# Kernel tuning notes

Measured on AMD Instinct MI355X. Metric: run time of the kernel, lower is better.

Reference implementation:

```python
import jax, jax.numpy as jnp
import numpy as np

N = 100_000      # nodes
E = 1_600_000    # edges
DIN = 128
DH = 128
DOUT = 2
BN_EPS = 1e-5


def setup_inputs() -> dict:
    key = jax.random.key(0)
    ks = jax.random.split(key, 14)
    s_in = 1.0 / np.sqrt(DIN)
    s_h = 1.0 / np.sqrt(DH)
    return {
        "x": jax.random.normal(ks[0], (N, DIN), jnp.float32),
        "edge_index": jax.random.randint(ks[1], (2, E), 0, N, jnp.int32),
        "W1": jax.random.normal(ks[2], (DIN, DH), jnp.float32) * s_in,
        "b1": jnp.zeros((DH,), jnp.float32),
        "W2": jax.random.normal(ks[3], (DH, DH), jnp.float32) * s_h,
        "b2": jnp.zeros((DH,), jnp.float32),
        "W3": jax.random.normal(ks[4], (DH, DH), jnp.float32) * s_h,
        "b3": jnp.zeros((DH,), jnp.float32),
        "gamma": jnp.ones((DH,), jnp.float32),
        "beta": jnp.zeros((DH,), jnp.float32),
        "Wc": jax.random.normal(ks[5], (DH, DH), jnp.float32) * s_h,
        "bc": jnp.zeros((DH,), jnp.float32),
        "Wr": jax.random.normal(ks[6], (DH, DOUT), jnp.float32) * s_h,
        "br": jnp.zeros((DOUT,), jnp.float32),
    }


def reference(x, edge_index, W1, b1, W2, b2, W3, b3, gamma, beta, Wc, bc, Wr, br):
    src, dst = edge_index[0], edge_index[1]
    # GCN symmetric normalization with self-loops (deg includes self-loop)
    deg = jnp.zeros((N,), x.dtype).at[dst].add(1.0) + 1.0
    dinv = jax.lax.rsqrt(deg)
    coef = (dinv[src] * dinv[dst])[:, None]        # [E,1]
    self_coef = (dinv * dinv)[:, None]             # [N,1] self-loop weight

    def gcn_conv(h, W, b):
        h = h @ W                                  # [N,DH] dense transform
        agg = jnp.zeros((N, h.shape[1]), h.dtype).at[dst].add(h[src] * coef)
        return agg + h * self_coef + b

    h = jax.nn.relu(gcn_conv(x, W1, b1))
    h = jax.nn.relu(gcn_conv(h, W2, b2))   # dropout is identity at inference
    h = jax.nn.relu(gcn_conv(h, W3, b3))
    # BatchNorm1d over the node dimension (training-mode batch statistics)
    mu = h.mean(axis=0)
    var = h.var(axis=0)
    h = (h - mu) * jax.lax.rsqrt(var + BN_EPS) * gamma + beta
    h = jax.nn.relu(h @ Wc + bc)
    return h @ Wr + br
```

## Files before the change

kernel.cpp:

```cpp
#include <hip/hip_runtime.h>

#define DHC 128
#define BSHIFT 8
#define BSIZE 256

typedef __attribute__((ext_vector_type(8))) __bf16 bf16x8;
typedef __attribute__((ext_vector_type(8))) unsigned short ushort8;
typedef __attribute__((ext_vector_type(4))) float floatx4;

__device__ inline unsigned short f2bf(float f) {
    unsigned int u = __float_as_uint(f);
    return (unsigned short)((u + 0x7FFFu + ((u >> 16) & 1u)) >> 16);
}
__device__ inline float bf2f_lo(unsigned int v) { return __uint_as_float(v << 16); }
__device__ inline float bf2f_hi(unsigned int v) { return __uint_as_float(v & 0xFFFF0000u); }


__global__ __launch_bounds__(256) void bucket_hist(const int* __restrict__ dst,
                                                   int* __restrict__ bcount, int e) {
    __shared__ int h[512];
    for (int i = threadIdx.x; i < 512; i += 256) h[i] = 0;
    __syncthreads();
    int base = blockIdx.x * 4096 + threadIdx.x;
#pragma unroll
    for (int j = 0; j < 16; j++) {
        int i = base + j * 256;
        if (i < e) atomicAdd(&h[dst[i] >> BSHIFT], 1);
    }
    __syncthreads();
    for (int i = threadIdx.x; i < 512; i += 256)
        if (h[i]) atomicAdd(&bcount[i], h[i]);
}

__global__ void bucket_scan(const int* __restrict__ bcount, int* __restrict__ bbase,
                            int* __restrict__ bcur, int* __restrict__ row_ptr,
                            int nb, int n, int e) {
    __shared__ int s[512];
    int t = threadIdx.x;
    s[t] = (t < nb) ? bcount[t] : 0;
    __syncthreads();
    for (int off = 1; off < 512; off <<= 1) {
        int add = (t >= off) ? s[t - off] : 0;
        __syncthreads();
        s[t] += add;
        __syncthreads();
    }
    if (t < nb) {
        int ex = (t == 0) ? 0 : s[t - 1];
        bbase[t] = ex;
        bcur[t] = ex;
    }
    if (t == 0) {
        bbase[nb] = e;
        row_ptr[n] = e;
    }
}

__global__ __launch_bounds__(256) void bucket_scatter(const int* __restrict__ src,
                                                      const int* __restrict__ dst,
                                                      int* __restrict__ bcur,
                                                      unsigned int* __restrict__ ebuf, int e) {
    __shared__ int h[512];
    __shared__ int rsv[512];
    for (int i = threadIdx.x; i < 512; i += 256) h[i] = 0;
    __syncthreads();
    int base = blockIdx.x * 4096 + threadIdx.x;
    int sreg[16], dreg[16];
#pragma unroll
    for (int j = 0; j < 16; j++) {
        int i = base + j * 256;
        if (i < e) {
            sreg[j] = src[i];
            dreg[j] = dst[i];
            atomicAdd(&h[dreg[j] >> BSHIFT], 1);
        } else {
            dreg[j] = -1;
        }
    }
    __syncthreads();
    for (int i = threadIdx.x; i < 512; i += 256) {
        int c = h[i];
        rsv[i] = c ? atomicAdd(&bcur[i], c) : 0;
        h[i] = 0;
    }
    __syncthreads();
#pragma unroll
    for (int j = 0; j < 16; j++) {
        if (dreg[j] >= 0) {
            int b = dreg[j] >> BSHIFT;
            int pos = rsv[b] + atomicAdd(&h[b], 1);
            ebuf[pos] = (unsigned int)sreg[j] | ((unsigned int)(dreg[j] & (BSIZE - 1)) << 20);
        }
    }
}

__global__ __launch_bounds__(256) void bucket_build(const unsigned int* __restrict__ ebuf,
                                                    const int* __restrict__ bbase,
                                                    int* __restrict__ row_ptr,
                                                    int* __restrict__ csr_src,
                                                    float* __restrict__ dinv,
                                                    float* __restrict__ selfc, int n) {
    __shared__ int ldeg[256];
    __shared__ int lcur[256];
    int b = blockIdx.x;
    int t = threadIdx.x;
    int beg = bbase[b], end = bbase[b + 1];
    ldeg[t] = 0;
    __syncthreads();
    for (int i = beg + t; i < end; i += 256) atomicAdd(&ldeg[ebuf[i] >> 20], 1);
    __syncthreads();
    int deg = ldeg[t];
    lcur[t] = deg;
    __syncthreads();
    for (int off = 1; off < 256; off <<= 1) {
        int add = (t >= off) ? lcur[t - off] : 0;
        __syncthreads();
        lcur[t] += add;
        __syncthreads();
    }
    int rp = beg + lcur[t] - deg;
    int node = (b << BSHIFT) + t;
    if (node < n) {
        row_ptr[node] = rp;
        float dv = rsqrtf((float)(deg + 1));
        dinv[node] = dv;
        selfc[node] = dv * dv;
    }
    __syncthreads();
    lcur[t] = rp;
    __syncthreads();
    for (int i = beg + t; i < end; i += 256) {
        unsigned int p = ebuf[i];
        int pos = atomicAdd(&lcur[p >> 20], 1);
        csr_src[pos] = (int)(p & 0xFFFFFu);
    }
}

__global__ void wconv3_k(const float* __restrict__ W1, const float* __restrict__ W2,
                         const float* __restrict__ W3, unsigned short* __restrict__ WTall) {
    int idx = blockIdx.x * 256 + threadIdx.x;
    int wsel = idx >> 14;
    int i = idx & 16383;
    int nn = i >> 7, k = i & 127;
    const float* W = (wsel == 0) ? W1 : (wsel == 1) ? W2 : W3;
    WTall[idx] = f2bf(W[k * 128 + nn]);
}

template <int MODE, int AF32>
__global__ __launch_bounds__(256, 2) void gemm_k(const void* __restrict__ Avoid,
                                                 const unsigned short* __restrict__ WT,
                                                 const float* __restrict__ bias,
                                                 unsigned short* __restrict__ outB,
                                                 float* __restrict__ outF,
                                                 const float* __restrict__ Wr,
                                                 const float* __restrict__ br, int n) {
    const int wave = threadIdx.x >> 6;
    const int lane = threadIdx.x & 63;
    const int m = lane & 15;
    const int kq = lane >> 4;

    bf16x8 bfrag[4][8];
#pragma unroll
    for (int ks = 0; ks < 4; ks++) {
        const int kb = ks * 32 + kq * 8;
#pragma unroll
        for (int ct = 0; ct < 8; ct++) {
            int nn = ct * 16 + m;
            bfrag[ks][ct] = __builtin_bit_cast(bf16x8, *(const ushort8*)(WT + nn * 128 + kb));
        }
    }

    const int rowbase = (blockIdx.x * 4 + wave) * 32;
    const int r0 = min(rowbase + m, n - 1);
    const int r1 = min(rowbase + 16 + m, n - 1);

    floatx4 acc[2][8];
#pragma unroll
    for (int rt = 0; rt < 2; rt++)
#pragma unroll
        for (int ct = 0; ct < 8; ct++) acc[rt][ct] = (floatx4){0.f, 0.f, 0.f, 0.f};

#pragma unroll
    for (int ks = 0; ks < 4; ks++) {
        const int kb = ks * 32 + kq * 8;
        bf16x8 a0, a1;
        if (AF32) {
            const float* Af = (const float*)Avoid;
            float4 f00 = *(const float4*)(Af + (size_t)r0 * 128 + kb);
            float4 f01 = *(const float4*)(Af + (size_t)r0 * 128 + kb + 4);
            float4 f10 = *(const float4*)(Af + (size_t)r1 * 128 + kb);
            float4 f11 = *(const float4*)(Af + (size_t)r1 * 128 + kb + 4);
            ushort8 u0, u1;
            u0[0] = f2bf(f00.x); u0[1] = f2bf(f00.y); u0[2] = f2bf(f00.z); u0[3] = f2bf(f00.w);
            u0[4] = f2bf(f01.x); u0[5] = f2bf(f01.y); u0[6] = f2bf(f01.z); u0[7] = f2bf(f01.w);
            u1[0] = f2bf(f10.x); u1[1] = f2bf(f10.y); u1[2] = f2bf(f10.z); u1[3] = f2bf(f10.w);
            u1[4] = f2bf(f11.x); u1[5] = f2bf(f11.y); u1[6] = f2bf(f11.z); u1[7] = f2bf(f11.w);
            a0 = __builtin_bit_cast(bf16x8, u0);
            a1 = __builtin_bit_cast(bf16x8, u1);
        } else {
            const unsigned short* Ab = (const unsigned short*)Avoid;
            a0 = __builtin_bit_cast(bf16x8, *(const ushort8*)(Ab + (size_t)r0 * 128 + kb));
            a1 = __builtin_bit_cast(bf16x8, *(const ushort8*)(Ab + (size_t)r1 * 128 + kb));
        }
#pragma unroll
        for (int ct = 0; ct < 8; ct++) {
            acc[0][ct] = __builtin_amdgcn_mfma_f32_16x16x32_bf16(a0, bfrag[ks][ct], acc[0][ct], 0, 0, 0);
            acc[1][ct] = __builtin_amdgcn_mfma_f32_16x16x32_bf16(a1, bfrag[ks][ct], acc[1][ct], 0, 0, 0);
        }
    }

    if (MODE == 0) {
#pragma unroll
        for (int rt = 0; rt < 2; rt++) {
#pragma unroll
            for (int ct = 0; ct < 8; ct++) {
                int col = ct * 16 + m;
#pragma unroll
                for (int i = 0; i < 4; i++) {
                    int r = rowbase + rt * 16 + kq * 4 + i;
                    if (r < n) outB[(size_t)r * 128 + col] = f2bf(acc[rt][ct][i]);
                }
            }
        }
    } else {
        float bcv[8], wr0[8], wr1[8];
#pragma unroll
        for (int ct = 0; ct < 8; ct++) {
            int col = ct * 16 + m;
            bcv[ct] = bias[col];
            float2 wv = ((const float2*)Wr)[col];
            wr0[ct] = wv.x;
            wr1[ct] = wv.y;
        }
        float br0 = br[0], br1 = br[1];
#pragma unroll
        for (int rt = 0; rt < 2; rt++) {
#pragma unroll
            for (int i = 0; i < 4; i++) {
                float p0 = 0.f, p1 = 0.f;
#pragma unroll
                for (int ct = 0; ct < 8; ct++) {
                    float v = fmaxf(acc[rt][ct][i] + bcv[ct], 0.f);
                    p0 = fmaf(v, wr0[ct], p0);
                    p1 = fmaf(v, wr1[ct], p1);
                }
#pragma unroll
                for (int mk = 1; mk < 16; mk <<= 1) {
                    p0 += __shfl_xor(p0, mk);
                    p1 += __shfl_xor(p1, mk);
                }
                int r = rowbase + rt * 16 + kq * 4 + i;
                if (m == 0 && r < n) ((float2*)outF)[r] = make_float2(p0 + br0, p1 + br1);
            }
        }
    }
}

__global__ __launch_bounds__(256) void agg_k(const unsigned short* __restrict__ hW,
                                             const int* __restrict__ csr,
                                             const int* __restrict__ row_ptr,
                                             const float* __restrict__ dinv,
                                             const float* __restrict__ selfc,
                                             const float* __restrict__ bias,
                                             unsigned short* __restrict__ out, int n) {
    int node = blockIdx.x * 4 + (threadIdx.x >> 6);
    int lane = threadIdx.x & 63;
    if (node >= n) return;
    int g = lane >> 4, t = lane & 15;
    int beg = row_ptr[node], end = row_ptr[node + 1];
    float dd = dinv[node];
    const uint4* h4 = (const uint4*)hW;
    float a[8];
#pragma unroll
    for (int i = 0; i < 8; i++) a[i] = 0.f;

    int len = end - beg;
    int q = (len + 3) >> 2;
    int e = beg + g * q;
    int e1 = min(e + q, end);

    for (; e + 3 < e1; e += 4) {
        int s0 = csr[e + 0], s1 = csr[e + 1], s2 = csr[e + 2], s3 = csr[e + 3];
        float c0 = dinv[s0] * dd, c1 = dinv[s1] * dd, c2 = dinv[s2] * dd, c3 = dinv[s3] * dd;
        uint4 v0 = h4[(size_t)s0 * 16 + t];
        uint4 v1 = h4[(size_t)s1 * 16 + t];
        uint4 v2 = h4[(size_t)s2 * 16 + t];
        uint4 v3 = h4[(size_t)s3 * 16 + t];
        a[0] = fmaf(c0, bf2f_lo(v0.x), a[0]); a[1] = fmaf(c0, bf2f_hi(v0.x), a[1]);
        a[2] = fmaf(c0, bf2f_lo(v0.y), a[2]); a[3] = fmaf(c0, bf2f_hi(v0.y), a[3]);
        a[4] = fmaf(c0, bf2f_lo(v0.z), a[4]); a[5] = fmaf(c0, bf2f_hi(v0.z), a[5]);
        a[6] = fmaf(c0, bf2f_lo(v0.w), a[6]); a[7] = fmaf(c0, bf2f_hi(v0.w), a[7]);
        a[0] = fmaf(c1, bf2f_lo(v1.x), a[0]); a[1] = fmaf(c1, bf2f_hi(v1.x), a[1]);
        a[2] = fmaf(c1, bf2f_lo(v1.y), a[2]); a[3] = fmaf(c1, bf2f_hi(v1.y), a[3]);
        a[4] = fmaf(c1, bf2f_lo(v1.z), a[4]); a[5] = fmaf(c1, bf2f_hi(v1.z), a[5]);
        a[6] = fmaf(c1, bf2f_lo(v1.w), a[6]); a[7] = fmaf(c1, bf2f_hi(v1.w), a[7]);
        a[0] = fmaf(c2, bf2f_lo(v2.x), a[0]); a[1] = fmaf(c2, bf2f_hi(v2.x), a[1]);
        a[2] = fmaf(c2, bf2f_lo(v2.y), a[2]); a[3] = fmaf(c2, bf2f_hi(v2.y), a[3]);
        a[4] = fmaf(c2, bf2f_lo(v2.z), a[4]); a[5] = fmaf(c2, bf2f_hi(v2.z), a[5]);
        a[6] = fmaf(c2, bf2f_lo(v2.w), a[6]); a[7] = fmaf(c2, bf2f_hi(v2.w), a[7]);
        a[0] = fmaf(c3, bf2f_lo(v3.x), a[0]); a[1] = fmaf(c3, bf2f_hi(v3.x), a[1]);
        a[2] = fmaf(c3, bf2f_lo(v3.y), a[2]); a[3] = fmaf(c3, bf2f_hi(v3.y), a[3]);
        a[4] = fmaf(c3, bf2f_lo(v3.z), a[4]); a[5] = fmaf(c3, bf2f_hi(v3.z), a[5]);
        a[6] = fmaf(c3, bf2f_lo(v3.w), a[6]); a[7] = fmaf(c3, bf2f_hi(v3.w), a[7]);
    }
    for (; e < e1; e++) {
        int s = csr[e];
        float c = dinv[s] * dd;
        uint4 v = h4[(size_t)s * 16 + t];
        a[0] = fmaf(c, bf2f_lo(v.x), a[0]); a[1] = fmaf(c, bf2f_hi(v.x), a[1]);
        a[2] = fmaf(c, bf2f_lo(v.y), a[2]); a[3] = fmaf(c, bf2f_hi(v.y), a[3]);
        a[4] = fmaf(c, bf2f_lo(v.z), a[4]); a[5] = fmaf(c, bf2f_hi(v.z), a[5]);
        a[6] = fmaf(c, bf2f_lo(v.w), a[6]); a[7] = fmaf(c, bf2f_hi(v.w), a[7]);
    }

    if (g == 0) {
        float sc = selfc[node];
        uint4 v = h4[(size_t)node * 16 + t];
        a[0] = fmaf(sc, bf2f_lo(v.x), a[0]); a[1] = fmaf(sc, bf2f_hi(v.x), a[1]);
        a[2] = fmaf(sc, bf2f_lo(v.y), a[2]); a[3] = fmaf(sc, bf2f_hi(v.y), a[3]);
        a[4] = fmaf(sc, bf2f_lo(v.z), a[4]); a[5] = fmaf(sc, bf2f_hi(v.z), a[5]);
        a[6] = fmaf(sc, bf2f_lo(v.w), a[6]); a[7] = fmaf(sc, bf2f_hi(v.w), a[7]);
    }
#pragma unroll
    for (int i = 0; i < 8; i++) {
        a[i] += __shfl_xor(a[i], 16);
        a[i] += __shfl_xor(a[i], 32);
    }
    if (g == 0) {
        float4 b0 = ((const float4*)bias)[t * 2];
        float4 b1 = ((const float4*)bias)[t * 2 + 1];
        uint4 o;
        o.x = (unsigned int)f2bf(fmaxf(a[0] + b0.x, 0.f)) |
              ((unsigned int)f2bf(fmaxf(a[1] + b0.y, 0.f)) << 16);
        o.y = (unsigned int)f2bf(fmaxf(a[2] + b0.z, 0.f)) |
              ((unsigned int)f2bf(fmaxf(a[3] + b0.w, 0.f)) << 16);
        o.z = (unsigned int)f2bf(fmaxf(a[4] + b1.x, 0.f)) |
              ((unsigned int)f2bf(fmaxf(a[5] + b1.y, 0.f)) << 16);
        o.w = (unsigned int)f2bf(fmaxf(a[6] + b1.z, 0.f)) |
              ((unsigned int)f2bf(fmaxf(a[7] + b1.w, 0.f)) << 16);
        ((uint4*)out)[(size_t)node * 16 + t] = o;
    }
}

__global__ __launch_bounds__(256) void bn_stats(const unsigned short* __restrict__ h,
                                                float* __restrict__ gsum,
                                                float* __restrict__ gsumsq, int n) {
    __shared__ float red[4][256];
    int l = threadIdx.x & 63;
    int rs = threadIdx.x >> 6;
    float s0 = 0.f, s1 = 0.f, q0 = 0.f, q1 = 0.f;
    for (int r = blockIdx.x * 4 + rs; r < n; r += gridDim.x * 4) {
        unsigned int v = *(const unsigned int*)(h + (size_t)r * 128 + l * 2);
        float a = bf2f_lo(v), b = bf2f_hi(v);
        s0 += a;
        s1 += b;
        q0 = fmaf(a, a, q0);
        q1 = fmaf(b, b, q1);
    }
    red[0][threadIdx.x] = s0;
    red[1][threadIdx.x] = s1;
    red[2][threadIdx.x] = q0;
    red[3][threadIdx.x] = q1;
    __syncthreads();
    if (threadIdx.x < 64) {
        float S0 = 0.f, S1 = 0.f, Q0 = 0.f, Q1 = 0.f;
#pragma unroll
        for (int j = 0; j < 4; j++) {
            S0 += red[0][j * 64 + l];
            S1 += red[1][j * 64 + l];
            Q0 += red[2][j * 64 + l];
            Q1 += red[3][j * 64 + l];
        }
        atomicAdd(&gsum[2 * l + 0], S0);
        atomicAdd(&gsum[2 * l + 1], S1);
        atomicAdd(&gsumsq[2 * l + 0], Q0);
        atomicAdd(&gsumsq[2 * l + 1], Q1);
    }
}

__global__ void bn_fold(const float* __restrict__ gsum, const float* __restrict__ gsumsq,
                        const float* __restrict__ gamma, const float* __restrict__ beta,
                        const float* __restrict__ Wc, const float* __restrict__ bc,
                        unsigned short* __restrict__ WcT, float* __restrict__ bcP, float invN) {
    __shared__ float scaleS[128], shiftS[128];
    int j = threadIdx.x;
    float mu = gsum[j] * invN;
    float var = gsumsq[j] * invN - mu * mu;
    float sc = gamma[j] * rsqrtf(var + 1e-5f);
    scaleS[j] = sc;
    shiftS[j] = beta[j] - mu * sc;
    __syncthreads();
    float accB = bc[j];
    for (int k = 0; k < 128; k++) {
        float w = Wc[k * 128 + j];
        WcT[j * 128 + k] = f2bf(scaleS[k] * w);
        accB = fmaf(shiftS[k], w, accB);
    }
    bcP[j] = accB;
}


extern "C" void kernel_launch(void* const* d_in, const int* in_sizes, int n_in,
                              void* d_out, int out_size, void* d_ws, size_t ws_size,
                              hipStream_t stream) {
    const float* x = (const float*)d_in[0];
    const int* ei = (const int*)d_in[1];
    const float* W1 = (const float*)d_in[2];
    const float* b1 = (const float*)d_in[3];
    const float* W2 = (const float*)d_in[4];
    const float* b2 = (const float*)d_in[5];
    const float* W3 = (const float*)d_in[6];
    const float* b3 = (const float*)d_in[7];
    const float* gamma = (const float*)d_in[8];
    const float* beta = (const float*)d_in[9];
    const float* Wc = (const float*)d_in[10];
    const float* bc = (const float*)d_in[11];
    const float* Wr = (const float*)d_in[12];
    const float* br = (const float*)d_in[13];
    float* out = (float*)d_out;

    const int N = in_sizes[0] / DHC;
    const int E = in_sizes[1] / 2;
    const int* srcIdx = ei;
    const int* dstIdx = ei + E;
    const int NB = (N + BSIZE - 1) >> BSHIFT;

    char* w = (char*)d_ws;
    size_t off = 0;
    auto alloc = [&](size_t bytes) -> void* {
        void* p = w + off;
        off += (bytes + 255) & ~(size_t)255;
        return p;
    };
    unsigned short* bufA = (unsigned short*)alloc((size_t)N * DHC * 2);
    unsigned short* bufB = (unsigned short*)alloc((size_t)N * DHC * 2);
    unsigned int* ebuf = (unsigned int*)alloc((size_t)E * 4);
    int* csr_src = (int*)alloc((size_t)E * 4);
    int* row_ptr = (int*)alloc((size_t)(N + 1) * 4);
    float* dinv = (float*)alloc((size_t)N * 4);
    float* selfc = (float*)alloc((size_t)N * 4);
    int* bcount = (int*)alloc(512 * 4 + 256 * 4);
    float* stats = (float*)(bcount + 512);
    float* gsum = stats;
    float* gsumsq = stats + 128;
    int* bbase = (int*)alloc(512 * 4);
    int* bcur = (int*)alloc(512 * 4);
    unsigned short* WTall = (unsigned short*)alloc((size_t)3 * 16384 * 2);
    unsigned short* WT1 = WTall;
    unsigned short* WT2 = WTall + 16384;
    unsigned short* WT3 = WTall + 32768;
    unsigned short* WcT = (unsigned short*)alloc(16384 * 2);
    float* bcP = (float*)alloc(128 * 4);
    (void)ws_size; (void)n_in; (void)out_size;

    hipMemsetAsync(bcount, 0, 512 * 4 + 256 * 4, stream);

    const int EB = (E + 4095) / 4096;
    bucket_hist<<<EB, 256, 0, stream>>>(dstIdx, bcount, E);
    bucket_scan<<<1, 512, 0, stream>>>(bcount, bbase, bcur, row_ptr, NB, N, E);
    bucket_scatter<<<EB, 256, 0, stream>>>(srcIdx, dstIdx, bcur, ebuf, E);
    bucket_build<<<NB, 256, 0, stream>>>(ebuf, bbase, row_ptr, csr_src, dinv, selfc, N);

    wconv3_k<<<192, 256, 0, stream>>>(W1, W2, W3, WTall);

    const int gemmBlocks = (N + 127) / 128;
    const int aggBlocks = (N + 3) / 4;

    gemm_k<0, 1><<<gemmBlocks, 256, 0, stream>>>(x, WT1, nullptr, bufB, nullptr, nullptr, nullptr, N);
    agg_k<<<aggBlocks, 256, 0, stream>>>(bufB, csr_src, row_ptr, dinv, selfc, b1, bufA, N);
    gemm_k<0, 0><<<gemmBlocks, 256, 0, stream>>>(bufA, WT2, nullptr, bufB, nullptr, nullptr, nullptr, N);
    agg_k<<<aggBlocks, 256, 0, stream>>>(bufB, csr_src, row_ptr, dinv, selfc, b2, bufA, N);
    gemm_k<0, 0><<<gemmBlocks, 256, 0, stream>>>(bufA, WT3, nullptr, bufB, nullptr, nullptr, nullptr, N);
    agg_k<<<aggBlocks, 256, 0, stream>>>(bufB, csr_src, row_ptr, dinv, selfc, b3, bufA, N);

    bn_stats<<<256, 256, 0, stream>>>(bufA, gsum, gsumsq, N);
    bn_fold<<<1, 128, 0, stream>>>(gsum, gsumsq, gamma, beta, Wc, bc, WcT, bcP, 1.0f / (float)N);
    gemm_k<2, 0><<<gemmBlocks, 256, 0, stream>>>(bufA, WcT, bcP, nullptr, out, Wr, br, N);
}
```

Measured before the change: 504.3 us.

## Stage GEMM weights in LDS and assign one node per 16-lane group in aggregation

The GEMM kernel no longer holds the full 128x128 weight fragment set in registers. It stages the weights in shared memory in MFMA-fragment order and reads them per k-step, which lowers register pressure so launch bounds can allow 4 blocks per CU. The aggregation kernel now processes 16 nodes per block, with each 16-lane group walking one node's whole edge list, instead of splitting each node's edges across four groups and combining them with cross-lane shuffles. This removes the shuffle reduction and the idle lanes on short rows, at the cost of longer serial loops on high-degree nodes and extra LDS traffic in the GEMM.

```diff
diff --git a/kernel.cpp b/kernel.cpp
--- a/kernel.cpp
+++ b/kernel.cpp
@@ -147,38 +147,39 @@
 }
 
 template <int MODE, int AF32>
-__global__ __launch_bounds__(256, 2) void gemm_k(const void* __restrict__ Avoid,
+__global__ __launch_bounds__(256, 4) void gemm_k(const void* __restrict__ Avoid,
                                                  const unsigned short* __restrict__ WT,
                                                  const float* __restrict__ bias,
                                                  unsigned short* __restrict__ outB,
                                                  float* __restrict__ outF,
                                                  const float* __restrict__ Wr,
                                                  const float* __restrict__ br, int n) {
+    __shared__ unsigned short Ws[32 * 512];
+    {
+        for (int c = threadIdx.x; c < 2048; c += 256) {
+            int f = c >> 6;
+            int l = c & 63;
+            int ks = f >> 3, ct = f & 7;
+            int nn = ct * 16 + (l & 15);
+            int kb = ks * 32 + (l >> 4) * 8;
+            *(uint4*)(&Ws[c * 8]) = *(const uint4*)(&WT[nn * 128 + kb]);
+        }
+    }
+    __syncthreads();
     const int wave = threadIdx.x >> 6;
     const int lane = threadIdx.x & 63;
+    const int rowbase = blockIdx.x * 128 + wave * 32;
     const int m = lane & 15;
     const int kq = lane >> 4;
 
-    bf16x8 bfrag[4][8];
-#pragma unroll
-    for (int ks = 0; ks < 4; ks++) {
-        const int kb = ks * 32 + kq * 8;
-#pragma unroll
-        for (int ct = 0; ct < 8; ct++) {
-            int nn = ct * 16 + m;
-            bfrag[ks][ct] = __builtin_bit_cast(bf16x8, *(const ushort8*)(WT + nn * 128 + kb));
-        }
-    }
-
-    const int rowbase = (blockIdx.x * 4 + wave) * 32;
+    floatx4 acc[2][8];
+#pragma unroll
+    for (int rt = 0; rt < 2; rt++)
+#pragma unroll
+        for (int ct = 0; ct < 8; ct++) acc[rt][ct] = (floatx4){0.f, 0.f, 0.f, 0.f};
+
     const int r0 = min(rowbase + m, n - 1);
     const int r1 = min(rowbase + 16 + m, n - 1);
-
-    floatx4 acc[2][8];
-#pragma unroll
-    for (int rt = 0; rt < 2; rt++)
-#pragma unroll
-        for (int ct = 0; ct < 8; ct++) acc[rt][ct] = (floatx4){0.f, 0.f, 0.f, 0.f};
 
 #pragma unroll
     for (int ks = 0; ks < 4; ks++) {
@@ -204,8 +205,10 @@
         }
 #pragma unroll
         for (int ct = 0; ct < 8; ct++) {
-            acc[0][ct] = __builtin_amdgcn_mfma_f32_16x16x32_bf16(a0, bfrag[ks][ct], acc[0][ct], 0, 0, 0);
-            acc[1][ct] = __builtin_amdgcn_mfma_f32_16x16x32_bf16(a1, bfrag[ks][ct], acc[1][ct], 0, 0, 0);
+            bf16x8 bfr = __builtin_bit_cast(bf16x8,
+                *(const ushort8*)(&Ws[(ks * 8 + ct) * 512 + lane * 8]));
+            acc[0][ct] = __builtin_amdgcn_mfma_f32_16x16x32_bf16(a0, bfr, acc[0][ct], 0, 0, 0);
+            acc[1][ct] = __builtin_amdgcn_mfma_f32_16x16x32_bf16(a1, bfr, acc[1][ct], 0, 0, 0);
         }
     }
 
@@ -263,10 +266,9 @@
                                              const float* __restrict__ selfc,
                                              const float* __restrict__ bias,
                                              unsigned short* __restrict__ out, int n) {
-    int node = blockIdx.x * 4 + (threadIdx.x >> 6);
-    int lane = threadIdx.x & 63;
+    int node = blockIdx.x * 16 + (threadIdx.x >> 4);
+    int t = threadIdx.x & 15;
     if (node >= n) return;
-    int g = lane >> 4, t = lane & 15;
     int beg = row_ptr[node], end = row_ptr[node + 1];
     float dd = dinv[node];
     const uint4* h4 = (const uint4*)hW;
@@ -274,12 +276,8 @@
 #pragma unroll
     for (int i = 0; i < 8; i++) a[i] = 0.f;
 
-    int len = end - beg;
-    int q = (len + 3) >> 2;
-    int e = beg + g * q;
-    int e1 = min(e + q, end);
-
-    for (; e + 3 < e1; e += 4) {
+    int e = beg;
+    for (; e + 3 < end; e += 4) {
         int s0 = csr[e + 0], s1 = csr[e + 1], s2 = csr[e + 2], s3 = csr[e + 3];
         float c0 = dinv[s0] * dd, c1 = dinv[s1] * dd, c2 = dinv[s2] * dd, c3 = dinv[s3] * dd;
         uint4 v0 = h4[(size_t)s0 * 16 + t];
@@ -303,7 +301,7 @@
         a[4] = fmaf(c3, bf2f_lo(v3.z), a[4]); a[5] = fmaf(c3, bf2f_hi(v3.z), a[5]);
         a[6] = fmaf(c3, bf2f_lo(v3.w), a[6]); a[7] = fmaf(c3, bf2f_hi(v3.w), a[7]);
     }
-    for (; e < e1; e++) {
+    for (; e < end; e++) {
         int s = csr[e];
         float c = dinv[s] * dd;
         uint4 v = h4[(size_t)s * 16 + t];
@@ -313,7 +311,7 @@
         a[6] = fmaf(c, bf2f_lo(v.w), a[6]); a[7] = fmaf(c, bf2f_hi(v.w), a[7]);
     }
 
-    if (g == 0) {
+    {
         float sc = selfc[node];
         uint4 v = h4[(size_t)node * 16 + t];
         a[0] = fmaf(sc, bf2f_lo(v.x), a[0]); a[1] = fmaf(sc, bf2f_hi(v.x), a[1]);
@@ -321,25 +319,18 @@
         a[4] = fmaf(sc, bf2f_lo(v.z), a[4]); a[5] = fmaf(sc, bf2f_hi(v.z), a[5]);
         a[6] = fmaf(sc, bf2f_lo(v.w), a[6]); a[7] = fmaf(sc, bf2f_hi(v.w), a[7]);
     }
-#pragma unroll
-    for (int i = 0; i < 8; i++) {
-        a[i] += __shfl_xor(a[i], 16);
-        a[i] += __shfl_xor(a[i], 32);
-    }
-    if (g == 0) {
-        float4 b0 = ((const float4*)bias)[t * 2];
-        float4 b1 = ((const float4*)bias)[t * 2 + 1];
-        uint4 o;
-        o.x = (unsigned int)f2bf(fmaxf(a[0] + b0.x, 0.f)) |
-              ((unsigned int)f2bf(fmaxf(a[1] + b0.y, 0.f)) << 16);
-        o.y = (unsigned int)f2bf(fmaxf(a[2] + b0.z, 0.f)) |
-              ((unsigned int)f2bf(fmaxf(a[3] + b0.w, 0.f)) << 16);
-        o.z = (unsigned int)f2bf(fmaxf(a[4] + b1.x, 0.f)) |
-              ((unsigned int)f2bf(fmaxf(a[5] + b1.y, 0.f)) << 16);
-        o.w = (unsigned int)f2bf(fmaxf(a[6] + b1.z, 0.f)) |
-              ((unsigned int)f2bf(fmaxf(a[7] + b1.w, 0.f)) << 16);
-        ((uint4*)out)[(size_t)node * 16 + t] = o;
-    }
+    float4 b0 = ((const float4*)bias)[t * 2];
+    float4 b1 = ((const float4*)bias)[t * 2 + 1];
+    uint4 o;
+    o.x = (unsigned int)f2bf(fmaxf(a[0] + b0.x, 0.f)) |
+          ((unsigned int)f2bf(fmaxf(a[1] + b0.y, 0.f)) << 16);
+    o.y = (unsigned int)f2bf(fmaxf(a[2] + b0.z, 0.f)) |
+          ((unsigned int)f2bf(fmaxf(a[3] + b0.w, 0.f)) << 16);
+    o.z = (unsigned int)f2bf(fmaxf(a[4] + b1.x, 0.f)) |
+          ((unsigned int)f2bf(fmaxf(a[5] + b1.y, 0.f)) << 16);
+    o.w = (unsigned int)f2bf(fmaxf(a[6] + b1.z, 0.f)) |
+          ((unsigned int)f2bf(fmaxf(a[7] + b1.w, 0.f)) << 16);
+    ((uint4*)out)[(size_t)node * 16 + t] = o;
 }
 
 __global__ __launch_bounds__(256) void bn_stats(const unsigned short* __restrict__ h,
@@ -464,7 +455,7 @@
     wconv3_k<<<192, 256, 0, stream>>>(W1, W2, W3, WTall);
 
     const int gemmBlocks = (N + 127) / 128;
-    const int aggBlocks = (N + 3) / 4;
+    const int aggBlocks = (N + 15) / 16;
 
     gemm_k<0, 1><<<gemmBlocks, 256, 0, stream>>>(x, WT1, nullptr, bufB, nullptr, nullptr, nullptr, N);
     agg_k<<<aggBlocks, 256, 0, stream>>>(bufB, csr_src, row_ptr, dinv, selfc, b1, bufA, N);
```

Result: faster. 455.8 us (-9.6%).
